# Optimization experiments

Hardware: AMD Instinct MI355X
Metric: run time of the kernel (lower is better)

The kernel has to match this reference:

```python
import jax, jax.numpy as jnp
import numpy as np

B, S, D_IN, D_HEAD = 4, 4096, 1024, 64

def setup_inputs() -> dict:
    key = jax.random.key(0)
    k1, k2, k3, k4 = jax.random.split(key, 4)
    scale = 0.02
    return {
        "input_vectors": jax.random.normal(k1, (B, S, D_IN), dtype=jnp.float32),
        "Wq": jax.random.normal(k2, (D_IN, D_HEAD), dtype=jnp.float32) * scale,
        "Wk": jax.random.normal(k3, (D_IN, D_HEAD), dtype=jnp.float32) * scale,
        "Wv": jax.random.normal(k4, (D_IN, D_HEAD), dtype=jnp.float32) * scale,
    }

def reference(input_vectors, Wq, Wk, Wv):
    # QKV projections (Linear with no bias): [B,S,d_in] @ [d_in,d_head]
    q = input_vectors @ Wq  # [B,S,H]
    k = input_vectors @ Wk
    v = input_vectors @ Wv
    n = input_vectors.shape[1]
    # causal attention scores: [B,S,S]
    scores = jnp.einsum('bqh,bkh->bqk', q, k)
    causal = jnp.tril(jnp.ones((n, n), dtype=bool))  # True = keep
    scores = jnp.where(causal, scores, -jnp.inf)
    scale = k.shape[-1] ** -0.5
    attn = jax.nn.softmax(scores * scale, axis=-1)
    return jnp.einsum('bqk,bkh->bqh', attn, v)
```

## Files before the change

### kernel.cpp

```cpp
#include <hip/hip_runtime.h>
#include <stdint.h>

#define SEQ   4096
#define DHEAD 64
#define DIN   1024

typedef __attribute__((ext_vector_type(8))) short bf16x8;
typedef __attribute__((ext_vector_type(4))) float floatx4;

#if __has_builtin(__builtin_amdgcn_exp2f)
#define EXP2(x) __builtin_amdgcn_exp2f(x)
#else
#define EXP2(x) exp2f(x)
#endif

__device__ __forceinline__ unsigned short f2bf(float f) {
    union { float f; unsigned int u; } v; v.f = f;
    unsigned int u = v.u + 0x7fffu + ((v.u >> 16) & 1u);
    return (unsigned short)(u >> 16);
}

__device__ __forceinline__ void g2l16(const void* g, const void* l) {
    __builtin_amdgcn_global_load_lds(
        (__attribute__((address_space(1))) unsigned int*)(uintptr_t)g,
        (__attribute__((address_space(3))) unsigned int*)(unsigned int)(uintptr_t)l,
        16, 0, 0);
}

__global__ void wt_prep(const float* __restrict__ Wq, const float* __restrict__ Wk,
                        const float* __restrict__ Wv, unsigned short* __restrict__ WT) {
    int idx = blockIdx.x * 256 + threadIdx.x;
    int k   = idx & 1023;
    int n   = (idx >> 10) & 63;
    int mat = idx >> 16;
    const float* W = (mat == 0) ? Wq : ((mat == 1) ? Wk : Wv);
    WT[idx] = f2bf(W[k * 64 + n]);
}

#define QSCALE 0.18033688011112042f
__launch_bounds__(256, 2)
__global__ void proj_qkv(const float* __restrict__ X, const unsigned short* __restrict__ WT,
                         unsigned short* __restrict__ qb, unsigned short* __restrict__ kb,
                         unsigned short* __restrict__ vb) {
    __shared__ __align__(16) float          Xl[32 * 64];
    __shared__ __align__(16) unsigned short Wl[192 * 64];
    const int tid = threadIdx.x;
    const int wave = tid >> 6, lane = tid & 63;
    const int quad = lane >> 4, l16 = lane & 15;
    const int strip = wave & 1, nh = wave >> 1;
    const int row0 = blockIdx.x * 32;
    const int m = strip * 16 + l16;

    floatx4 acc[6];
#pragma unroll
    for (int i = 0; i < 6; i++) acc[i] = (floatx4){0.f, 0.f, 0.f, 0.f};

    for (int kc = 0; kc < 16; kc++) {
        const int k0 = kc * 64;
        __syncthreads();
#pragma unroll
        for (int i = 0; i < 2; i++) {
            int u = (wave * 2 + i) * 64 + lane;
            int r = u >> 4, cp = u & 15, c = cp ^ (r & 15);
            g2l16(X + (size_t)(row0 + r) * DIN + k0 + c * 4, &Xl[u * 4]);
        }
#pragma unroll
        for (int it = 0; it < 6; it++) {
            int u = (wave * 6 + it) * 64 + lane;
            int r = u >> 3, cp = u & 7, c = cp ^ (r & 7);
            g2l16(WT + (size_t)r * 1024 + k0 + c * 8, &Wl[u * 8]);
        }
        __syncthreads();
        bf16x8 af[2];
#pragma unroll
        for (int ks = 0; ks < 2; ks++) {
            floatx4 x0 = *(const floatx4*)&Xl[m * 64 + ((ks * 8 + quad * 2 + 0) ^ (m & 15)) * 4];
            floatx4 x1 = *(const floatx4*)&Xl[m * 64 + ((ks * 8 + quad * 2 + 1) ^ (m & 15)) * 4];
#pragma unroll
            for (int j = 0; j < 4; j++) {
                af[ks][j]     = (short)f2bf(x0[j]);
                af[ks][j + 4] = (short)f2bf(x1[j]);
            }
        }
#pragma unroll
        for (int i = 0; i < 6; i++) {
            const int nrow = (nh * 6 + i) * 16 + l16;
#pragma unroll
            for (int ks = 0; ks < 2; ks++) {
                const int c = ks * 4 + quad;
                bf16x8 bfrag = *(const bf16x8*)&Wl[nrow * 64 + (c ^ (nrow & 7)) * 8];
                acc[i] = __builtin_amdgcn_mfma_f32_16x16x32_bf16(af[ks], bfrag, acc[i], 0, 0, 0);
            }
        }
    }
    const int orow0 = row0 + strip * 16;
#pragma unroll
    for (int i = 0; i < 6; i++) {
        const int nt = nh * 6 + i;
        const int mat = nt >> 2;
        const int col = (nt & 3) * 16 + l16;
#pragma unroll
        for (int r = 0; r < 4; r++) {
            const int orow = orow0 + quad * 4 + r;
            float v = acc[i][r];
            if (mat == 0) {
                qb[(size_t)orow * 64 + col] = f2bf(v * QSCALE);
            } else if (mat == 1) {
                kb[(size_t)orow * 64 + col] = f2bf(v);
            } else {
                int b = orow >> 12, s = orow & 4095;
                vb[((size_t)b * 64 + col) * SEQ + s] = f2bf(v);
            }
        }
    }
}

__launch_bounds__(256, 2)
__global__ void attn(const unsigned short* __restrict__ qb, const unsigned short* __restrict__ kb,
                     const unsigned short* __restrict__ vb, float* __restrict__ out) {
    __shared__ __align__(16) unsigned short Kl[128 * 64];
    __shared__ __align__(16) unsigned short Vl[64 * 128];
    __shared__ __align__(16) unsigned short Pl[4][16 * 72];
    __shared__ float Ll[2][16][16];
    float* Ol = (float*)Kl;

    const int bid = blockIdx.x;
    const int batch = bid & 3;
    const int qt = 127 - (bid >> 2);
    const int q0 = qt * 32;
    const int tid = threadIdx.x;
    const int wave = tid >> 6, lane = tid & 63;
    const int quad = lane >> 4, l16 = lane & 15;
    const int strip = wave & 1, kh = wave >> 1;

    const unsigned short* qrow = qb + (size_t)(batch * SEQ + q0 + strip * 16 + l16) * 64;
    bf16x8 qa[2];
    qa[0] = *(const bf16x8*)(qrow + quad * 8);
    qa[1] = *(const bf16x8*)(qrow + 32 + quad * 8);

    floatx4 o[4];
#pragma unroll
    for (int i = 0; i < 4; i++) o[i] = (floatx4){0.f, 0.f, 0.f, 0.f};
    float lrow[4] = {0.f, 0.f, 0.f, 0.f};

    const unsigned short* kbase = kb + (size_t)batch * SEQ * 64;
    const unsigned short* vbase = vb + (size_t)batch * 64 * SEQ;
    const int T = (q0 + 32 + 127) >> 7;

    for (int kt = 0; kt < T; kt++) {
        const int k0 = kt * 128;
        __syncthreads();
#pragma unroll
        for (int i = 0; i < 4; i++) {
            int u = (wave * 4 + i) * 64 + lane;
            int r = u >> 3, cp = u & 7, c = cp ^ (r & 7);
            g2l16(kbase + (size_t)(k0 + r) * 64 + c * 8, &Kl[u * 8]);
        }
#pragma unroll
        for (int i = 0; i < 4; i++) {
            int u = (wave * 4 + i) * 64 + lane;
            int d = u >> 4, cp = u & 15, c = cp ^ (d & 15);
            g2l16(vbase + (size_t)d * SEQ + k0 + c * 8, &Vl[u * 8]);
        }
        __syncthreads();

        floatx4 sc[4];
#pragma unroll
        for (int nt = 0; nt < 4; nt++) {
            sc[nt] = (floatx4){0.f, 0.f, 0.f, 0.f};
            const int key = kh * 64 + nt * 16 + l16;
#pragma unroll
            for (int ks = 0; ks < 2; ks++) {
                const int c = ks * 4 + quad;
                bf16x8 bk = *(const bf16x8*)&Kl[key * 64 + (c ^ (key & 7)) * 8];
                sc[nt] = __builtin_amdgcn_mfma_f32_16x16x32_bf16(qa[ks], bk, sc[nt], 0, 0, 0);
            }
        }
        if (kt == T - 1) {
#pragma unroll
            for (int nt = 0; nt < 4; nt++) {
                const int col = k0 + kh * 64 + nt * 16 + l16;
#pragma unroll
                for (int r = 0; r < 4; r++) {
                    const int rowg = q0 + strip * 16 + quad * 4 + r;
                    if (col > rowg) sc[nt][r] = -1e30f;
                }
            }
        }
        unsigned short* P = &Pl[wave][0];
#pragma unroll
        for (int r = 0; r < 4; r++) {
#pragma unroll
            for (int nt = 0; nt < 4; nt++) {
                float p = EXP2(sc[nt][r]);
                lrow[r] += p;
                P[(quad * 4 + r) * 72 + nt * 16 + l16] = f2bf(p);
            }
        }
        bf16x8 pa[2];
        pa[0] = *(const bf16x8*)&P[l16 * 72 + quad * 8];
        pa[1] = *(const bf16x8*)&P[l16 * 72 + 32 + quad * 8];
#pragma unroll
        for (int nt = 0; nt < 4; nt++) {
            const int d = nt * 16 + l16;
#pragma unroll
            for (int ks = 0; ks < 2; ks++) {
                const int c = kh * 8 + ks * 4 + quad;
                bf16x8 bv = *(const bf16x8*)&Vl[d * 128 + (c ^ (d & 15)) * 8];
                o[nt] = __builtin_amdgcn_mfma_f32_16x16x32_bf16(pa[ks], bv, o[nt], 0, 0, 0);
            }
        }
    }

    __syncthreads();
    if (kh == 1) {
#pragma unroll
        for (int nt = 0; nt < 4; nt++)
#pragma unroll
            for (int r = 0; r < 4; r++)
                Ol[strip * 1024 + (quad * 4 + r) * 64 + nt * 16 + l16] = o[nt][r];
#pragma unroll
        for (int r = 0; r < 4; r++) Ll[strip][quad * 4 + r][l16] = lrow[r];
    }
    __syncthreads();
    if (kh == 0) {
#pragma unroll
        for (int nt = 0; nt < 4; nt++)
#pragma unroll
            for (int r = 0; r < 4; r++)
                o[nt][r] += Ol[strip * 1024 + (quad * 4 + r) * 64 + nt * 16 + l16];
        float* ob = out + (size_t)(batch * SEQ + q0 + strip * 16) * 64;
#pragma unroll
        for (int r = 0; r < 4; r++) {
            float l = lrow[r] + Ll[strip][quad * 4 + r][l16];
            l += __shfl_xor(l, 1);
            l += __shfl_xor(l, 2);
            l += __shfl_xor(l, 4);
            l += __shfl_xor(l, 8);
            const float inv = 1.f / l;
#pragma unroll
            for (int nt = 0; nt < 4; nt++)
                ob[(quad * 4 + r) * 64 + nt * 16 + l16] = o[nt][r] * inv;
        }
    }
}

extern "C" void kernel_launch(void* const* d_in, const int* in_sizes, int n_in,
                              void* d_out, int out_size, void* d_ws, size_t ws_size,
                              hipStream_t stream) {
    const float* X  = (const float*)d_in[0];
    const float* Wq = (const float*)d_in[1];
    const float* Wk = (const float*)d_in[2];
    const float* Wv = (const float*)d_in[3];
    float* out = (float*)d_out;
    char* ws = (char*)d_ws;
    unsigned short* WT = (unsigned short*)ws;
    unsigned short* qb = (unsigned short*)(ws + 393216);
    unsigned short* kb = (unsigned short*)(ws + 393216 + 2097152);
    unsigned short* vb = (unsigned short*)(ws + 393216 + 2 * 2097152);

    hipLaunchKernelGGL(wt_prep,  dim3(768), dim3(256), 0, stream, Wq, Wk, Wv, WT);
    hipLaunchKernelGGL(proj_qkv, dim3(512), dim3(256), 0, stream, X, WT, qb, kb, vb);
    hipLaunchKernelGGL(attn,     dim3(512), dim3(256), 0, stream, qb, kb, vb, out);
}
```

Measured before the change: 153.0 us.

## Double-buffer LDS tiles in projection and attention kernels to overlap loads

Both the QKV projection and the attention kernel now keep two LDS buffers. The next tile is loaded with global_load_lds while the current tile is being computed, so each iteration needs one barrier instead of two and memory latency can hide behind MFMA work. The attention kernel also changes its block-to-query-tile order: the second half of the grid now walks light tiles in ascending order. The cost is double the LDS footprint, which could limit occupancy, and the new ordering may shift load balance.

```diff
diff --git a/kernel.cpp b/kernel.cpp
--- a/kernel.cpp
+++ b/kernel.cpp
@@ -42,8 +42,8 @@
 __global__ void proj_qkv(const float* __restrict__ X, const unsigned short* __restrict__ WT,
                          unsigned short* __restrict__ qb, unsigned short* __restrict__ kb,
                          unsigned short* __restrict__ vb) {
-    __shared__ __align__(16) float          Xl[32 * 64];
-    __shared__ __align__(16) unsigned short Wl[192 * 64];
+    __shared__ __align__(16) float          X0[32 * 64], X1[32 * 64];
+    __shared__ __align__(16) unsigned short W0[192 * 64], W1[192 * 64];
     const int tid = threadIdx.x;
     const int wave = tid >> 6, lane = tid & 63;
     const int quad = lane >> 4, l16 = lane & 15;
@@ -55,27 +55,26 @@
 #pragma unroll
     for (int i = 0; i < 6; i++) acc[i] = (floatx4){0.f, 0.f, 0.f, 0.f};
 
-    for (int kc = 0; kc < 16; kc++) {
-        const int k0 = kc * 64;
-        __syncthreads();
+    auto stage = [&](float* Xd, unsigned short* Wd, int k0) {
 #pragma unroll
         for (int i = 0; i < 2; i++) {
             int u = (wave * 2 + i) * 64 + lane;
             int r = u >> 4, cp = u & 15, c = cp ^ (r & 15);
-            g2l16(X + (size_t)(row0 + r) * DIN + k0 + c * 4, &Xl[u * 4]);
-        }
-#pragma unroll
-        for (int it = 0; it < 6; it++) {
-            int u = (wave * 6 + it) * 64 + lane;
+            g2l16(X + (size_t)(row0 + r) * DIN + k0 + c * 4, Xd + u * 4);
+        }
+#pragma unroll
+        for (int i = 0; i < 6; i++) {
+            int u = (wave * 6 + i) * 64 + lane;
             int r = u >> 3, cp = u & 7, c = cp ^ (r & 7);
-            g2l16(WT + (size_t)r * 1024 + k0 + c * 8, &Wl[u * 8]);
-        }
-        __syncthreads();
+            g2l16(WT + (size_t)r * 1024 + k0 + c * 8, Wd + u * 8);
+        }
+    };
+    auto compute = [&](const float* Xs, const unsigned short* Ws) {
         bf16x8 af[2];
 #pragma unroll
         for (int ks = 0; ks < 2; ks++) {
-            floatx4 x0 = *(const floatx4*)&Xl[m * 64 + ((ks * 8 + quad * 2 + 0) ^ (m & 15)) * 4];
-            floatx4 x1 = *(const floatx4*)&Xl[m * 64 + ((ks * 8 + quad * 2 + 1) ^ (m & 15)) * 4];
+            floatx4 x0 = *(const floatx4*)&Xs[m * 64 + ((ks * 8 + quad * 2 + 0) ^ (m & 15)) * 4];
+            floatx4 x1 = *(const floatx4*)&Xs[m * 64 + ((ks * 8 + quad * 2 + 1) ^ (m & 15)) * 4];
 #pragma unroll
             for (int j = 0; j < 4; j++) {
                 af[ks][j]     = (short)f2bf(x0[j]);
@@ -88,11 +87,22 @@
 #pragma unroll
             for (int ks = 0; ks < 2; ks++) {
                 const int c = ks * 4 + quad;
-                bf16x8 bfrag = *(const bf16x8*)&Wl[nrow * 64 + (c ^ (nrow & 7)) * 8];
+                bf16x8 bfrag = *(const bf16x8*)&Ws[nrow * 64 + (c ^ (nrow & 7)) * 8];
                 acc[i] = __builtin_amdgcn_mfma_f32_16x16x32_bf16(af[ks], bfrag, acc[i], 0, 0, 0);
             }
         }
-    }
+    };
+
+    stage(X0, W0, 0);
+    for (int kc = 0; kc < 16; kc += 2) {
+        __syncthreads();
+        if (kc + 1 < 16) stage(X1, W1, (kc + 1) * 64);
+        compute(X0, W0);
+        __syncthreads();
+        if (kc + 2 < 16) stage(X0, W0, (kc + 2) * 64);
+        compute(X1, W1);
+    }
+
     const int orow0 = row0 + strip * 16;
 #pragma unroll
     for (int i = 0; i < 6; i++) {
@@ -118,15 +128,16 @@
 __launch_bounds__(256, 2)
 __global__ void attn(const unsigned short* __restrict__ qb, const unsigned short* __restrict__ kb,
                      const unsigned short* __restrict__ vb, float* __restrict__ out) {
-    __shared__ __align__(16) unsigned short Kl[128 * 64];
-    __shared__ __align__(16) unsigned short Vl[64 * 128];
+    __shared__ __align__(16) unsigned short K0[128 * 64], K1[128 * 64];
+    __shared__ __align__(16) unsigned short V0[64 * 128], V1[64 * 128];
     __shared__ __align__(16) unsigned short Pl[4][16 * 72];
     __shared__ float Ll[2][16][16];
-    float* Ol = (float*)Kl;
+    float* Ol = (float*)K0;
 
     const int bid = blockIdx.x;
-    const int batch = bid & 3;
-    const int qt = 127 - (bid >> 2);
+    int qt, batch;
+    if (bid < 256) { qt = 127 - (bid >> 2); batch = bid & 3; }
+    else           { qt = (bid - 256) >> 2; batch = bid & 3; }
     const int q0 = qt * 32;
     const int tid = threadIdx.x;
     const int wave = tid >> 6, lane = tid & 63;
@@ -147,23 +158,21 @@
     const unsigned short* vbase = vb + (size_t)batch * 64 * SEQ;
     const int T = (q0 + 32 + 127) >> 7;
 
-    for (int kt = 0; kt < T; kt++) {
-        const int k0 = kt * 128;
-        __syncthreads();
+    auto stage = [&](unsigned short* Kd, unsigned short* Vd, int k0) {
 #pragma unroll
         for (int i = 0; i < 4; i++) {
             int u = (wave * 4 + i) * 64 + lane;
             int r = u >> 3, cp = u & 7, c = cp ^ (r & 7);
-            g2l16(kbase + (size_t)(k0 + r) * 64 + c * 8, &Kl[u * 8]);
+            g2l16(kbase + (size_t)(k0 + r) * 64 + c * 8, Kd + u * 8);
         }
 #pragma unroll
         for (int i = 0; i < 4; i++) {
             int u = (wave * 4 + i) * 64 + lane;
             int d = u >> 4, cp = u & 15, c = cp ^ (d & 15);
-            g2l16(vbase + (size_t)d * SEQ + k0 + c * 8, &Vl[u * 8]);
-        }
-        __syncthreads();
-
+            g2l16(vbase + (size_t)d * SEQ + k0 + c * 8, Vd + u * 8);
+        }
+    };
+    auto compute = [&](const unsigned short* Ks, const unsigned short* Vs, int k0, bool last) {
         floatx4 sc[4];
 #pragma unroll
         for (int nt = 0; nt < 4; nt++) {
@@ -172,11 +181,11 @@
 #pragma unroll
             for (int ks = 0; ks < 2; ks++) {
                 const int c = ks * 4 + quad;
-                bf16x8 bk = *(const bf16x8*)&Kl[key * 64 + (c ^ (key & 7)) * 8];
+                bf16x8 bk = *(const bf16x8*)&Ks[key * 64 + (c ^ (key & 7)) * 8];
                 sc[nt] = __builtin_amdgcn_mfma_f32_16x16x32_bf16(qa[ks], bk, sc[nt], 0, 0, 0);
             }
         }
-        if (kt == T - 1) {
+        if (last) {
 #pragma unroll
             for (int nt = 0; nt < 4; nt++) {
                 const int col = k0 + kh * 64 + nt * 16 + l16;
@@ -206,10 +215,21 @@
 #pragma unroll
             for (int ks = 0; ks < 2; ks++) {
                 const int c = kh * 8 + ks * 4 + quad;
-                bf16x8 bv = *(const bf16x8*)&Vl[d * 128 + (c ^ (d & 15)) * 8];
+                bf16x8 bv = *(const bf16x8*)&Vs[d * 128 + (c ^ (d & 15)) * 8];
                 o[nt] = __builtin_amdgcn_mfma_f32_16x16x32_bf16(pa[ks], bv, o[nt], 0, 0, 0);
             }
         }
+    };
+
+    stage(K0, V0, 0);
+    for (int kt = 0; kt < T; kt += 2) {
+        __syncthreads();
+        if (kt + 1 < T) stage(K1, V1, (kt + 1) * 128);
+        compute(K0, V0, kt * 128, kt == T - 1);
+        if (kt + 1 >= T) break;
+        __syncthreads();
+        if (kt + 2 < T) stage(K0, V0, (kt + 2) * 128);
+        compute(K1, V1, (kt + 1) * 128, kt + 1 == T - 1);
     }
 
     __syncthreads();
```

Result: faster. 144.7 us (-5.4%).

## Split attention key range across two blocks and merge partials; halve projection tile

Applied to the files above, without the earlier changes.

The attention kernel now splits each query tile's key range into two halves handled by separate blocks. Each block writes its unnormalized partial output and row sums, and a new merge kernel adds the two partials and normalizes. This is possible because there is no running max, so partials add directly. The change doubles grid size to fill more CUs and balance causal work. The projection kernel uses 16-row tiles with 4 waves each covering 3 output tiles, doubling its block count, and both kernels raise launch bounds occupancy. It costs extra global traffic for partials and an additional kernel launch.

```diff
diff --git a/kernel.cpp b/kernel.cpp
--- a/kernel.cpp
+++ b/kernel.cpp
@@ -38,44 +38,42 @@
 }
 
 #define QSCALE 0.18033688011112042f
-__launch_bounds__(256, 2)
+__launch_bounds__(256, 4)
 __global__ void proj_qkv(const float* __restrict__ X, const unsigned short* __restrict__ WT,
                          unsigned short* __restrict__ qb, unsigned short* __restrict__ kb,
                          unsigned short* __restrict__ vb) {
-    __shared__ __align__(16) float          Xl[32 * 64];
+    __shared__ __align__(16) float          Xl[16 * 64];
     __shared__ __align__(16) unsigned short Wl[192 * 64];
     const int tid = threadIdx.x;
     const int wave = tid >> 6, lane = tid & 63;
     const int quad = lane >> 4, l16 = lane & 15;
-    const int strip = wave & 1, nh = wave >> 1;
-    const int row0 = blockIdx.x * 32;
-    const int m = strip * 16 + l16;
-
-    floatx4 acc[6];
-#pragma unroll
-    for (int i = 0; i < 6; i++) acc[i] = (floatx4){0.f, 0.f, 0.f, 0.f};
+    const int row0 = blockIdx.x * 16;
+    const int m = l16;
+
+    floatx4 acc[3];
+#pragma unroll
+    for (int i = 0; i < 3; i++) acc[i] = (floatx4){0.f, 0.f, 0.f, 0.f};
 
     for (int kc = 0; kc < 16; kc++) {
         const int k0 = kc * 64;
         __syncthreads();
-#pragma unroll
-        for (int i = 0; i < 2; i++) {
-            int u = (wave * 2 + i) * 64 + lane;
+        {
+            int u = tid;
             int r = u >> 4, cp = u & 15, c = cp ^ (r & 15);
-            g2l16(X + (size_t)(row0 + r) * DIN + k0 + c * 4, &Xl[u * 4]);
-        }
-#pragma unroll
-        for (int it = 0; it < 6; it++) {
-            int u = (wave * 6 + it) * 64 + lane;
+            g2l16(X + (size_t)(row0 + r) * DIN + k0 + c * 4, Xl + u * 4);
+        }
+#pragma unroll
+        for (int i = 0; i < 6; i++) {
+            int u = (wave * 6 + i) * 64 + lane;
             int r = u >> 3, cp = u & 7, c = cp ^ (r & 7);
-            g2l16(WT + (size_t)r * 1024 + k0 + c * 8, &Wl[u * 8]);
+            g2l16(WT + (size_t)r * 1024 + k0 + c * 8, Wl + u * 8);
         }
         __syncthreads();
         bf16x8 af[2];
 #pragma unroll
         for (int ks = 0; ks < 2; ks++) {
-            floatx4 x0 = *(const floatx4*)&Xl[m * 64 + ((ks * 8 + quad * 2 + 0) ^ (m & 15)) * 4];
-            floatx4 x1 = *(const floatx4*)&Xl[m * 64 + ((ks * 8 + quad * 2 + 1) ^ (m & 15)) * 4];
+            floatx4 x0 = *(const floatx4*)&Xl[m * 64 + ((ks * 8 + quad * 2 + 0) ^ m) * 4];
+            floatx4 x1 = *(const floatx4*)&Xl[m * 64 + ((ks * 8 + quad * 2 + 1) ^ m) * 4];
 #pragma unroll
             for (int j = 0; j < 4; j++) {
                 af[ks][j]     = (short)f2bf(x0[j]);
@@ -83,8 +81,8 @@
             }
         }
 #pragma unroll
-        for (int i = 0; i < 6; i++) {
-            const int nrow = (nh * 6 + i) * 16 + l16;
+        for (int i = 0; i < 3; i++) {
+            const int nrow = (wave * 3 + i) * 16 + l16;
 #pragma unroll
             for (int ks = 0; ks < 2; ks++) {
                 const int c = ks * 4 + quad;
@@ -93,15 +91,14 @@
             }
         }
     }
-    const int orow0 = row0 + strip * 16;
-#pragma unroll
-    for (int i = 0; i < 6; i++) {
-        const int nt = nh * 6 + i;
+#pragma unroll
+    for (int i = 0; i < 3; i++) {
+        const int nt = wave * 3 + i;
         const int mat = nt >> 2;
         const int col = (nt & 3) * 16 + l16;
 #pragma unroll
         for (int r = 0; r < 4; r++) {
-            const int orow = orow0 + quad * 4 + r;
+            const int orow = row0 + quad * 4 + r;
             float v = acc[i][r];
             if (mat == 0) {
                 qb[(size_t)orow * 64 + col] = f2bf(v * QSCALE);
@@ -115,9 +112,10 @@
     }
 }
 
-__launch_bounds__(256, 2)
+__launch_bounds__(256, 4)
 __global__ void attn(const unsigned short* __restrict__ qb, const unsigned short* __restrict__ kb,
-                     const unsigned short* __restrict__ vb, float* __restrict__ out) {
+                     const unsigned short* __restrict__ vb, float* __restrict__ opart,
+                     float* __restrict__ lpart) {
     __shared__ __align__(16) unsigned short Kl[128 * 64];
     __shared__ __align__(16) unsigned short Vl[64 * 128];
     __shared__ __align__(16) unsigned short Pl[4][16 * 72];
@@ -125,14 +123,23 @@
     float* Ol = (float*)Kl;
 
     const int bid = blockIdx.x;
-    const int batch = bid & 3;
-    const int qt = 127 - (bid >> 2);
+    const int hkb   = bid & 1;
+    const int batch = (bid >> 1) & 3;
+    const int qidx  = bid >> 3;
+    const int h = (qidx >> 5) & 1;
+    const int f = (qidx & 31) | ((qidx >> 6) << 5);
+    const int qt = h ? 127 - f : f;
     const int q0 = qt * 32;
     const int tid = threadIdx.x;
     const int wave = tid >> 6, lane = tid & 63;
     const int quad = lane >> 4, l16 = lane & 15;
     const int strip = wave & 1, kh = wave >> 1;
 
+    const int Tfull = (q0 + 32 + 127) >> 7;
+    const int T0 = (Tfull + 1) >> 1;
+    const int ktlo = hkb ? T0 : 0;
+    const int kthi = hkb ? Tfull : T0;
+
     const unsigned short* qrow = qb + (size_t)(batch * SEQ + q0 + strip * 16 + l16) * 64;
     bf16x8 qa[2];
     qa[0] = *(const bf16x8*)(qrow + quad * 8);
@@ -145,22 +152,21 @@
 
     const unsigned short* kbase = kb + (size_t)batch * SEQ * 64;
     const unsigned short* vbase = vb + (size_t)batch * 64 * SEQ;
-    const int T = (q0 + 32 + 127) >> 7;
-
-    for (int kt = 0; kt < T; kt++) {
+
+    for (int kt = ktlo; kt < kthi; kt++) {
         const int k0 = kt * 128;
         __syncthreads();
 #pragma unroll
         for (int i = 0; i < 4; i++) {
             int u = (wave * 4 + i) * 64 + lane;
             int r = u >> 3, cp = u & 7, c = cp ^ (r & 7);
-            g2l16(kbase + (size_t)(k0 + r) * 64 + c * 8, &Kl[u * 8]);
+            g2l16(kbase + (size_t)(k0 + r) * 64 + c * 8, Kl + u * 8);
         }
 #pragma unroll
         for (int i = 0; i < 4; i++) {
             int u = (wave * 4 + i) * 64 + lane;
             int d = u >> 4, cp = u & 15, c = cp ^ (d & 15);
-            g2l16(vbase + (size_t)d * SEQ + k0 + c * 8, &Vl[u * 8]);
+            g2l16(vbase + (size_t)d * SEQ + k0 + c * 8, Vl + u * 8);
         }
         __syncthreads();
 
@@ -176,7 +182,7 @@
                 sc[nt] = __builtin_amdgcn_mfma_f32_16x16x32_bf16(qa[ks], bk, sc[nt], 0, 0, 0);
             }
         }
-        if (kt == T - 1) {
+        if (kt == Tfull - 1) {
 #pragma unroll
             for (int nt = 0; nt < 4; nt++) {
                 const int col = k0 + kh * 64 + nt * 16 + l16;
@@ -229,7 +235,10 @@
 #pragma unroll
             for (int r = 0; r < 4; r++)
                 o[nt][r] += Ol[strip * 1024 + (quad * 4 + r) * 64 + nt * 16 + l16];
-        float* ob = out + (size_t)(batch * SEQ + q0 + strip * 16) * 64;
+        float* ob = opart + (size_t)hkb * (4 * SEQ * 64)
+                  + (size_t)(batch * SEQ + q0 + strip * 16) * 64;
+        float* lb = lpart + (size_t)hkb * (4 * SEQ)
+                  + (size_t)(batch * SEQ + q0 + strip * 16);
 #pragma unroll
         for (int r = 0; r < 4; r++) {
             float l = lrow[r] + Ll[strip][quad * 4 + r][l16];
@@ -237,12 +246,23 @@
             l += __shfl_xor(l, 2);
             l += __shfl_xor(l, 4);
             l += __shfl_xor(l, 8);
-            const float inv = 1.f / l;
 #pragma unroll
             for (int nt = 0; nt < 4; nt++)
-                ob[(quad * 4 + r) * 64 + nt * 16 + l16] = o[nt][r] * inv;
-        }
-    }
+                ob[(quad * 4 + r) * 64 + nt * 16 + l16] = o[nt][r];
+            if (l16 == 0) lb[quad * 4 + r] = l;
+        }
+    }
+}
+
+__global__ void merge(const float* __restrict__ opart, const float* __restrict__ lpart,
+                      float* __restrict__ out) {
+    int idx = blockIdx.x * 256 + threadIdx.x;
+    int row = idx >> 4, c4 = idx & 15;
+    floatx4 a = *(const floatx4*)(opart + (size_t)row * 64 + c4 * 4);
+    floatx4 b = *(const floatx4*)(opart + (size_t)(4 * SEQ * 64) + (size_t)row * 64 + c4 * 4);
+    float inv = 1.f / (lpart[row] + lpart[4 * SEQ + row]);
+    floatx4 r = (a + b) * inv;
+    *(floatx4*)(out + (size_t)row * 64 + c4 * 4) = r;
 }
 
 extern "C" void kernel_launch(void* const* d_in, const int* in_sizes, int n_in,
@@ -258,8 +278,11 @@
     unsigned short* qb = (unsigned short*)(ws + 393216);
     unsigned short* kb = (unsigned short*)(ws + 393216 + 2097152);
     unsigned short* vb = (unsigned short*)(ws + 393216 + 2 * 2097152);
-
-    hipLaunchKernelGGL(wt_prep,  dim3(768), dim3(256), 0, stream, Wq, Wk, Wv, WT);
-    hipLaunchKernelGGL(proj_qkv, dim3(512), dim3(256), 0, stream, X, WT, qb, kb, vb);
-    hipLaunchKernelGGL(attn,     dim3(512), dim3(256), 0, stream, qb, kb, vb, out);
-}
+    float* opart = (float*)(ws + 393216 + 3 * 2097152);
+    float* lpart = (float*)(ws + 393216 + 3 * 2097152 + 8388608);
+
+    hipLaunchKernelGGL(wt_prep,  dim3(768),  dim3(256), 0, stream, Wq, Wk, Wv, WT);
+    hipLaunchKernelGGL(proj_qkv, dim3(1024), dim3(256), 0, stream, X, WT, qb, kb, vb);
+    hipLaunchKernelGGL(attn,     dim3(1024), dim3(256), 0, stream, qb, kb, vb, opart, lpart);
+    hipLaunchKernelGGL(merge,    dim3(1024), dim3(256), 0, stream, opart, lpart, out);
+}
```

Result: no change. 152.0 us (-0.6%).
